# Kernel tuning notes

Hardware: AMD Instinct MI355X
Metric: run time of the kernel (lower is better)

The kernel has to match this reference:

```python
import jax, jax.numpy as jnp
import numpy as np

N_HEADS, D_MODEL, D_HEAD = 16, 1024, 64
BATCH, SEQ = 2, 2048
INIT_RANGE = 0.02


def setup_inputs() -> dict:
    key = jax.random.key(0)
    ks = jax.random.split(key, 5)
    x = jax.random.normal(ks[0], (BATCH, SEQ, D_MODEL), dtype=jnp.float32)
    W_Q = jax.random.normal(ks[1], (N_HEADS, D_MODEL, D_HEAD), dtype=jnp.float32) * INIT_RANGE
    W_K = jax.random.normal(ks[2], (N_HEADS, D_MODEL, D_HEAD), dtype=jnp.float32) * INIT_RANGE
    W_V = jax.random.normal(ks[3], (N_HEADS, D_MODEL, D_HEAD), dtype=jnp.float32) * INIT_RANGE
    W_O = jax.random.normal(ks[4], (N_HEADS, D_HEAD, D_MODEL), dtype=jnp.float32) * INIT_RANGE
    b_Q = jnp.zeros((N_HEADS, D_HEAD), dtype=jnp.float32)
    b_K = jnp.zeros((N_HEADS, D_HEAD), dtype=jnp.float32)
    b_V = jnp.zeros((N_HEADS, D_HEAD), dtype=jnp.float32)
    b_O = jnp.zeros((D_MODEL,), dtype=jnp.float32)
    return {"normalized_resid_pre": x, "W_Q": W_Q, "W_K": W_K, "W_V": W_V,
            "W_O": W_O, "b_Q": b_Q, "b_K": b_K, "b_V": b_V, "b_O": b_O}


def reference(normalized_resid_pre, W_Q, W_K, W_V, W_O, b_Q, b_K, b_V, b_O):
    x = normalized_resid_pre  # [b, s, d_model]
    q = jnp.einsum('bsm,hmd->bshd', x, W_Q) + b_Q  # [b, s, h, d_head]
    k = jnp.einsum('bsm,hmd->bshd', x, W_K) + b_K
    v = jnp.einsum('bsm,hmd->bshd', x, W_V) + b_V
    scores = jnp.einsum('bqhd,bkhd->bhqk', q, k) / jnp.sqrt(jnp.float32(D_HEAD))
    seq = x.shape[1]
    causal = jnp.tril(jnp.ones((seq, seq), dtype=bool))  # True where allowed
    scores = jnp.where(causal, scores, jnp.float32(-jnp.inf))
    pattern = jax.nn.softmax(scores, axis=-1)  # [b, h, q, k]
    z = jnp.einsum('bhqk,bkhd->bqhd', pattern, v)
    attn_out = jnp.einsum('bqhd,hdm->bqm', z, W_O) + b_O
    return attn_out
```

## Files before the change

kernel.cpp:

```cpp
#include <hip/hip_runtime.h>
#include <hip/hip_bf16.h>

#define BATCH 2
#define SEQL 2048
#define NH 16
#define DH 64
#define DM 1024
#define LDK 72
#define QSCALE 0.1803368801111244f

typedef __hip_bfloat16 bf16;
typedef __attribute__((ext_vector_type(8))) short  bf16x8;
typedef __attribute__((ext_vector_type(4))) float  f32x4;

__device__ __forceinline__ void gl_lds16(const void* g, void* l) {
    __builtin_amdgcn_global_load_lds(
        (const __attribute__((address_space(1))) unsigned int*)g,
        (__attribute__((address_space(3))) unsigned int*)l, 16, 0, 0);
}

__global__ __launch_bounds__(256) void prep_kernel(
    const float* __restrict__ x,
    const float* __restrict__ Wq, const float* __restrict__ Wk,
    const float* __restrict__ Wv, const float* __restrict__ Wo,
    bf16* __restrict__ Wt, bf16* __restrict__ xb)
{
    const int zi = blockIdx.z;
    if (zi == 4) {
        const int bid = blockIdx.y * 16 + blockIdx.x;
        const size_t base = ((size_t)bid * 256 + threadIdx.x) * 4;
        #pragma unroll
        for (int it = 0; it < 16; ++it) {
            const size_t i = base + (size_t)it * 262144;
            const float4 v = *(const float4*)(x + i);
            bf16 o[4];
            o[0] = __float2bfloat16(v.x); o[1] = __float2bfloat16(v.y);
            o[2] = __float2bfloat16(v.z); o[3] = __float2bfloat16(v.w);
            *(uint2*)(xb + i) = *(const uint2*)o;
        }
        return;
    }

    __shared__ float ts[64][65];
    const float* src = (zi == 0) ? Wq : (zi == 1) ? Wk : (zi == 2) ? Wv : Wo;
    bf16* dst = Wt + (size_t)zi * DM * DM;
    const int row0 = blockIdx.y * 64;
    const int col0 = blockIdx.x * 64;
    const int tx = threadIdx.x & 63;
    const int ty = threadIdx.x >> 6;

    if (zi < 3) {
        const int h = col0 >> 6;
        #pragma unroll
        for (int i = 0; i < 16; ++i) {
            const int r = ty + 4 * i;
            ts[r][tx] = src[h * (DM * DH) + (row0 + r) * DH + tx];
        }
    } else {
        #pragma unroll
        for (int i = 0; i < 16; ++i) {
            const int r = ty + 4 * i;
            ts[r][tx] = src[(size_t)(row0 + r) * DM + col0 + tx];
        }
    }
    __syncthreads();
    #pragma unroll
    for (int i = 0; i < 16; ++i) {
        const int rr = ty + 4 * i;
        dst[(size_t)(col0 + rr) * DM + row0 + tx] = __float2bfloat16(ts[tx][rr]);
    }
}

__global__ __launch_bounds__(256) void qkv_gemm(
    const bf16* __restrict__ xb, const bf16* __restrict__ Wt,
    const float* __restrict__ bq, const float* __restrict__ bk, const float* __restrict__ bv,
    bf16* __restrict__ qkv)
{
    __shared__ __align__(16) bf16 As[2][128 * 32];
    __shared__ __align__(16) bf16 Bs[2][128 * 32];

    const int t = threadIdx.x;
    const int lane = t & 63, w = t >> 6;
    const int ml = lane & 15, quad = lane >> 4;
    const int wr = w >> 1, wc = w & 1;
    const int bn = blockIdx.x, bm = blockIdx.y, which = blockIdx.z;

    const bf16* A0 = xb + (size_t)(bm * 128) * DM;
    const bf16* B0 = Wt + (size_t)which * DM * DM + (size_t)(bn * 128) * DM;
    const float* bias = (which == 0) ? bq : (which == 1) ? bk : bv;
    bf16* outb = qkv + (size_t)which * (BATCH * SEQL * NH * DH);
    const float oscale = (which == 0) ? QSCALE : 1.0f;

    f32x4 acc[4][4];
    #pragma unroll
    for (int i = 0; i < 4; ++i)
        #pragma unroll
        for (int j = 0; j < 4; ++j) acc[i][j] = (f32x4){0.f, 0.f, 0.f, 0.f};

    const int r0 = t >> 2, c0 = (t & 3) * 8;
    const int f1 = t + 256;
    const int r1 = f1 >> 2, c1 = (f1 & 3) * 8;

    for (int kt = 0; kt < DM / 64; ++kt) {
        const int k0 = kt * 64;
        __syncthreads();
        #pragma unroll
        for (int half = 0; half < 2; ++half) {
            const int kh = k0 + half * 32;
            gl_lds16(A0 + (size_t)r0 * DM + kh + c0, &As[half][t * 8]);
            gl_lds16(A0 + (size_t)r1 * DM + kh + c1, &As[half][f1 * 8]);
            gl_lds16(B0 + (size_t)r0 * DM + kh + c0, &Bs[half][t * 8]);
            gl_lds16(B0 + (size_t)r1 * DM + kh + c1, &Bs[half][f1 * 8]);
        }
        __syncthreads();
        #pragma unroll
        for (int half = 0; half < 2; ++half) {
            bf16x8 af[4], bfr[4];
            #pragma unroll
            for (int i = 0; i < 4; ++i)
                af[i] = *(const bf16x8*)&As[half][(wr * 64 + i * 16 + ml) * 32 + quad * 8];
            #pragma unroll
            for (int j = 0; j < 4; ++j)
                bfr[j] = *(const bf16x8*)&Bs[half][(wc * 64 + j * 16 + ml) * 32 + quad * 8];
            #pragma unroll
            for (int i = 0; i < 4; ++i)
                #pragma unroll
                for (int j = 0; j < 4; ++j)
                    acc[i][j] = __builtin_amdgcn_mfma_f32_16x16x32_bf16(af[i], bfr[j], acc[i][j], 0, 0, 0);
        }
    }

    float bb[4];
    #pragma unroll
    for (int j = 0; j < 4; ++j) bb[j] = bias[bn * 128 + wc * 64 + j * 16 + ml];

    if (which == 2) {
        #pragma unroll
        for (int i = 0; i < 4; ++i) {
            const int row0v = bm * 128 + wr * 64 + i * 16 + quad * 4;
            const int b = row0v >> 11;
            const int s0 = row0v & (SEQL - 1);
            #pragma unroll
            for (int j = 0; j < 4; ++j) {
                const int col = bn * 128 + wc * 64 + j * 16 + ml;
                const int h = col >> 6, d = col & 63;
                bf16 tmp[4];
                #pragma unroll
                for (int rg = 0; rg < 4; ++rg)
                    tmp[rg] = __float2bfloat16(acc[i][j][rg] + bb[j]);
                *(uint2*)&outb[(((size_t)(b * NH + h)) * DH + d) * SEQL + s0] =
                    *(const uint2*)tmp;
            }
        }
    } else {
        #pragma unroll
        for (int i = 0; i < 4; ++i) {
            #pragma unroll
            for (int rg = 0; rg < 4; ++rg) {
                const int row = bm * 128 + wr * 64 + i * 16 + quad * 4 + rg;
                const int b = row >> 11;
                const int s = row & (SEQL - 1);
                #pragma unroll
                for (int j = 0; j < 4; ++j) {
                    const int col = bn * 128 + wc * 64 + j * 16 + ml;
                    const int h = col >> 6, d = col & 63;
                    outb[(((size_t)(b * NH + h)) * SEQL + s) * DH + d] =
                        __float2bfloat16((acc[i][j][rg] + bb[j]) * oscale);
                }
            }
        }
    }
}

__global__ __launch_bounds__(256) void oproj_gemm(
    const bf16* __restrict__ zb, const bf16* __restrict__ Bt,
    const float* __restrict__ bo, float* __restrict__ out)
{
    __shared__ __align__(16) bf16 As[2][128 * 32];
    __shared__ __align__(16) bf16 Bs[2][64 * 32];

    const int t = threadIdx.x;
    const int lane = t & 63, w = t >> 6;
    const int ml = lane & 15, quad = lane >> 4;
    const int wr = w >> 1, wc = w & 1;
    const int bn = blockIdx.x, bm = blockIdx.y;

    const bf16* A0 = zb + (size_t)(bm * 128) * DM;
    const bf16* B0 = Bt + (size_t)(bn * 64) * DM;

    f32x4 acc[4][2];
    #pragma unroll
    for (int i = 0; i < 4; ++i)
        #pragma unroll
        for (int j = 0; j < 2; ++j) acc[i][j] = (f32x4){0.f, 0.f, 0.f, 0.f};

    const int r0 = t >> 2, c0 = (t & 3) * 8;
    const int f1 = t + 256;
    const int r1 = f1 >> 2, c1 = (f1 & 3) * 8;

    for (int kt = 0; kt < DM / 64; ++kt) {
        const int k0 = kt * 64;
        __syncthreads();
        #pragma unroll
        for (int half = 0; half < 2; ++half) {
            const int kh = k0 + half * 32;
            gl_lds16(A0 + (size_t)r0 * DM + kh + c0, &As[half][t * 8]);
            gl_lds16(A0 + (size_t)r1 * DM + kh + c1, &As[half][f1 * 8]);
            gl_lds16(B0 + (size_t)r0 * DM + kh + c0, &Bs[half][t * 8]);
        }
        __syncthreads();
        #pragma unroll
        for (int half = 0; half < 2; ++half) {
            bf16x8 af[4], bfr[2];
            #pragma unroll
            for (int i = 0; i < 4; ++i)
                af[i] = *(const bf16x8*)&As[half][(wr * 64 + i * 16 + ml) * 32 + quad * 8];
            #pragma unroll
            for (int j = 0; j < 2; ++j)
                bfr[j] = *(const bf16x8*)&Bs[half][(wc * 32 + j * 16 + ml) * 32 + quad * 8];
            #pragma unroll
            for (int i = 0; i < 4; ++i)
                #pragma unroll
                for (int j = 0; j < 2; ++j)
                    acc[i][j] = __builtin_amdgcn_mfma_f32_16x16x32_bf16(af[i], bfr[j], acc[i][j], 0, 0, 0);
        }
    }

    float bb[2];
    #pragma unroll
    for (int j = 0; j < 2; ++j) bb[j] = bo[bn * 64 + wc * 32 + j * 16 + ml];

    #pragma unroll
    for (int i = 0; i < 4; ++i) {
        #pragma unroll
        for (int rg = 0; rg < 4; ++rg) {
            const int row = bm * 128 + wr * 64 + i * 16 + quad * 4 + rg;
            #pragma unroll
            for (int j = 0; j < 2; ++j) {
                const int col = bn * 64 + wc * 32 + j * 16 + ml;
                out[(size_t)row * DM + col] = acc[i][j][rg] + bb[j];
            }
        }
    }
}

__global__ __launch_bounds__(512) void attn_kernel(
    const bf16* __restrict__ qg, const bf16* __restrict__ kg, const bf16* __restrict__ vtg,
    bf16* __restrict__ z)
{
    __shared__ __align__(16) bf16 KsS[64 * 64];
    __shared__ __align__(16) bf16 VtS[64 * 64];
    __shared__ __align__(16) bf16 PsS[8][16 * LDK];

    const int t    = threadIdx.x;
    const int lane = t & 63;
    const int w    = t >> 6;
    const int m    = lane & 15;
    const int quad = lane >> 4;
    const int wg   = w & 3;
    const int half = w >> 2;

    const int bh = blockIdx.x;
    const int b  = bh >> 4;
    const int h  = bh & 15;
    const int qa = blockIdx.y;
    const int qb = 31 - qa;
    const int q0a = qa * 64;
    const int q0b = qb * 64;

    const size_t base   = (size_t)bh * SEQL * DH;
    const size_t vtbase = (size_t)bh * DH * SEQL;

    const int s  = t;
    const int rs = s >> 3, cs = (s & 7) ^ (rs & 7);

    bf16x8 aq[2], aqB[2];
    {
        const int myq = (w < 4) ? (q0a + w * 16) : (q0b + wg * 16);
        const bf16* qp = qg + base + (size_t)(myq + m) * DH + quad * 8;
        aq[0] = *(const bf16x8*)(qp);
        aq[1] = *(const bf16x8*)(qp + 32);
        const bf16* qpb = qg + base + (size_t)(q0b + wg * 16 + m) * DH + quad * 8;
        aqB[0] = *(const bf16x8*)(qpb);
        aqB[1] = *(const bf16x8*)(qpb + 32);
    }

    const short ob = (m == 0) ? (short)0x3F80 : (short)0;
    const bf16x8 bones = {ob, ob, ob, ob, ob, ob, ob, ob};

    f32x4 zacc[4];
    #pragma unroll
    for (int nt = 0; nt < 4; ++nt) zacc[nt] = (f32x4){0.f, 0.f, 0.f, 0.f};
    f32x4 lacc = (f32x4){0.f, 0.f, 0.f, 0.f};

    bf16* Psw = PsS[w];

    for (int kt = 0; kt <= qb; ++kt) {
        __syncthreads();
        {
            const int kc = kt * 64;
            gl_lds16(kg + base + (size_t)(kc + rs) * DH + cs * 8, &KsS[s * 8]);
            gl_lds16(vtg + vtbase + (size_t)rs * SEQL + kc + cs * 8, &VtS[s * 8]);
        }
        __syncthreads();

        if (kt <= qa) {
            f32x4 sc[4];
            #pragma unroll
            for (int nt = 0; nt < 4; ++nt) sc[nt] = (f32x4){0.f, 0.f, 0.f, 0.f};
            __builtin_amdgcn_s_setprio(1);
            #pragma unroll
            for (int ks = 0; ks < 2; ++ks) {
                #pragma unroll
                for (int nt = 0; nt < 4; ++nt) {
                    const int row = nt * 16 + m;
                    const int pc  = ((ks << 2) + quad) ^ (m & 7);
                    const bf16x8 bk = *(const bf16x8*)(&KsS[row * 64 + pc * 8]);
                    sc[nt] = __builtin_amdgcn_mfma_f32_16x16x32_bf16(aq[ks], bk, sc[nt], 0, 0, 0);
                }
            }
            __builtin_amdgcn_s_setprio(0);
            if (kt == qa && w < 4) {
                #pragma unroll
                for (int nt = 0; nt < 4; ++nt) {
                    const int col = nt * 16 + m;
                    #pragma unroll
                    for (int rg = 0; rg < 4; ++rg) {
                        const int row = wg * 16 + quad * 4 + rg;
                        if (col > row) sc[nt][rg] = -1e30f;
                    }
                }
            }

            #pragma unroll
            for (int nt = 0; nt < 4; ++nt)
                #pragma unroll
                for (int rg = 0; rg < 4; ++rg)
                    Psw[(quad * 4 + rg) * LDK + nt * 16 + m] =
                        __float2bfloat16(__builtin_exp2f(sc[nt][rg]));

            __builtin_amdgcn_s_setprio(1);
            #pragma unroll
            for (int ks = 0; ks < 2; ++ks) {
                const bf16x8 ap = *(const bf16x8*)(&Psw[m * LDK + ks * 32 + quad * 8]);
                lacc = __builtin_amdgcn_mfma_f32_16x16x32_bf16(ap, bones, lacc, 0, 0, 0);
                #pragma unroll
                for (int nt = 0; nt < 4; ++nt) {
                    const int row = nt * 16 + m;
                    const int pc  = ((ks << 2) + quad) ^ (m & 7);
                    const bf16x8 bv = *(const bf16x8*)(&VtS[row * 64 + pc * 8]);
                    zacc[nt] = __builtin_amdgcn_mfma_f32_16x16x32_bf16(ap, bv, zacc[nt], 0, 0, 0);
                }
            }
            __builtin_amdgcn_s_setprio(0);

            if (kt == qa && w < 4) {
                float invl[4];
                #pragma unroll
                for (int rg = 0; rg < 4; ++rg)
                    invl[rg] = 1.f / __shfl(lacc[rg], quad * 16);
                #pragma unroll
                for (int nt = 0; nt < 4; ++nt) {
                    const int d = nt * 16 + m;
                    #pragma unroll
                    for (int rg = 0; rg < 4; ++rg) {
                        const int qrow = q0a + wg * 16 + quad * 4 + rg;
                        z[(((size_t)b * SEQL + qrow) * NH + h) * DH + d] =
                            __float2bfloat16(zacc[nt][rg] * invl[rg]);
                    }
                }
                #pragma unroll
                for (int nt = 0; nt < 4; ++nt) zacc[nt] = (f32x4){0.f, 0.f, 0.f, 0.f};
                lacc = (f32x4){0.f, 0.f, 0.f, 0.f};
                aq[0] = aqB[0]; aq[1] = aqB[1];
            }
        } else {
            f32x4 sc[2];
            sc[0] = (f32x4){0.f, 0.f, 0.f, 0.f};
            sc[1] = (f32x4){0.f, 0.f, 0.f, 0.f};
            __builtin_amdgcn_s_setprio(1);
            #pragma unroll
            for (int ks = 0; ks < 2; ++ks) {
                #pragma unroll
                for (int nt = 0; nt < 2; ++nt) {
                    const int row = half * 32 + nt * 16 + m;
                    const int pc  = ((ks << 2) + quad) ^ (m & 7);
                    const bf16x8 bk = *(const bf16x8*)(&KsS[row * 64 + pc * 8]);
                    sc[nt] = __builtin_amdgcn_mfma_f32_16x16x32_bf16(aq[ks], bk, sc[nt], 0, 0, 0);
                }
            }
            __builtin_amdgcn_s_setprio(0);
            if (kt == qb) {
                #pragma unroll
                for (int nt = 0; nt < 2; ++nt) {
                    const int col = half * 32 + nt * 16 + m;
                    #pragma unroll
                    for (int rg = 0; rg < 4; ++rg) {
                        const int row = wg * 16 + quad * 4 + rg;
                        if (col > row) sc[nt][rg] = -1e30f;
                    }
                }
            }

            #pragma unroll
            for (int nt = 0; nt < 2; ++nt)
                #pragma unroll
                for (int rg = 0; rg < 4; ++rg)
                    Psw[(quad * 4 + rg) * LDK + nt * 16 + m] =
                        __float2bfloat16(__builtin_exp2f(sc[nt][rg]));

            __builtin_amdgcn_s_setprio(1);
            {
                const bf16x8 ap = *(const bf16x8*)(&Psw[m * LDK + quad * 8]);
                lacc = __builtin_amdgcn_mfma_f32_16x16x32_bf16(ap, bones, lacc, 0, 0, 0);
                #pragma unroll
                for (int nt = 0; nt < 4; ++nt) {
                    const int row = nt * 16 + m;
                    const int pc  = ((half << 2) + quad) ^ (m & 7);
                    const bf16x8 bv = *(const bf16x8*)(&VtS[row * 64 + pc * 8]);
                    zacc[nt] = __builtin_amdgcn_mfma_f32_16x16x32_bf16(ap, bv, zacc[nt], 0, 0, 0);
                }
            }
            __builtin_amdgcn_s_setprio(0);
        }
    }

    __syncthreads();
    if (w < 4) {
        float* zs = (w < 2) ? ((float*)KsS) + (size_t)w * 1024
                            : ((float*)VtS) + (size_t)(w - 2) * 1024;
        #pragma unroll
        for (int nt = 0; nt < 4; ++nt)
            #pragma unroll
            for (int rg = 0; rg < 4; ++rg)
                zs[lane * 16 + nt * 4 + rg] = zacc[nt][rg];
        float* ls = ((float*)PsS) + w * 256;
        #pragma unroll
        for (int rg = 0; rg < 4; ++rg) ls[lane * 4 + rg] = lacc[rg];
    }
    __syncthreads();
    if (w >= 4) {
        const int ww = w - 4;
        const float* zs = (ww < 2) ? ((const float*)KsS) + (size_t)ww * 1024
                                   : ((const float*)VtS) + (size_t)(ww - 2) * 1024;
        const float* ls = ((const float*)PsS) + ww * 256;
        #pragma unroll
        for (int nt = 0; nt < 4; ++nt)
            #pragma unroll
            for (int rg = 0; rg < 4; ++rg)
                zacc[nt][rg] += zs[lane * 16 + nt * 4 + rg];
        #pragma unroll
        for (int rg = 0; rg < 4; ++rg) lacc[rg] += ls[lane * 4 + rg];

        float invl[4];
        #pragma unroll
        for (int rg = 0; rg < 4; ++rg)
            invl[rg] = 1.f / __shfl(lacc[rg], quad * 16);
        #pragma unroll
        for (int nt = 0; nt < 4; ++nt) {
            const int d = nt * 16 + m;
            #pragma unroll
            for (int rg = 0; rg < 4; ++rg) {
                const int qrow = q0b + wg * 16 + quad * 4 + rg;
                z[(((size_t)b * SEQL + qrow) * NH + h) * DH + d] =
                    __float2bfloat16(zacc[nt][rg] * invl[rg]);
            }
        }
    }
}

extern "C" void kernel_launch(void* const* d_in, const int* in_sizes, int n_in,
                              void* d_out, int out_size, void* d_ws, size_t ws_size,
                              hipStream_t stream)
{
    const float* x  = (const float*)d_in[0];
    const float* Wq = (const float*)d_in[1];
    const float* Wk = (const float*)d_in[2];
    const float* Wv = (const float*)d_in[3];
    const float* Wo = (const float*)d_in[4];
    const float* bq = (const float*)d_in[5];
    const float* bk = (const float*)d_in[6];
    const float* bv = (const float*)d_in[7];
    const float* bo = (const float*)d_in[8];
    float* out = (float*)d_out;

    const size_t TOK = (size_t)BATCH * SEQL;
    const size_t QKV = TOK * DM;
    bf16* xb  = (bf16*)d_ws;
    bf16* Wt  = xb + QKV;
    bf16* qkv = Wt + 4 * (size_t)DM * DM;
    bf16* zb  = qkv + 3 * QKV;

    prep_kernel<<<dim3(16, 16, 5), 256, 0, stream>>>(x, Wq, Wk, Wv, Wo, Wt, xb);
    qkv_gemm<<<dim3(8, 32, 3), 256, 0, stream>>>(xb, Wt, bq, bk, bv, qkv);
    attn_kernel<<<dim3(BATCH * NH, 16), 512, 0, stream>>>(
        qkv, qkv + QKV, qkv + 2 * QKV, zb);
    oproj_gemm<<<dim3(16, 32), 256, 0, stream>>>(zb, Wt + 3 * (size_t)DM * DM, bo, out);
}
```

Measured before the change: 184.8 us.

## Restructure QKV GEMM into 256x256 tiles with pipelined swizzled LDS staging

Rewrites the QKV projection GEMM to use 512-thread blocks computing 256x256 output tiles over the concatenated QKV weight. K-slices are staged two ahead into XOR-swizzled LDS buffers, loads are interleaved between MFMA phases, and setprio is raised around the MFMA sections. The block index is remapped so that neighbouring blocks share A and B tiles. The aim is more operand reuse per LDS load, fewer bank conflicts and overlap of global loads with compute, at the cost of much higher register and LDS use (64KB per block) and only 192 blocks launched.

```diff
diff --git a/kernel.cpp b/kernel.cpp
--- a/kernel.cpp
+++ b/kernel.cpp
@@ -10,8 +10,8 @@
 #define QSCALE 0.1803368801111244f
 
 typedef __hip_bfloat16 bf16;
-typedef __attribute__((ext_vector_type(8))) short  bf16x8;
-typedef __attribute__((ext_vector_type(4))) float  f32x4;
+typedef __attribute__((ext_vector_type(8)))  short bf16x8;
+typedef __attribute__((ext_vector_type(4)))  float f32x4;
 
 __device__ __forceinline__ void gl_lds16(const void* g, void* l) {
     __builtin_amdgcn_global_load_lds(
@@ -71,104 +71,195 @@
     }
 }
 
-__global__ __launch_bounds__(256) void qkv_gemm(
+__global__ __launch_bounds__(512, 2) void qkv_gemm(
     const bf16* __restrict__ xb, const bf16* __restrict__ Wt,
     const float* __restrict__ bq, const float* __restrict__ bk, const float* __restrict__ bv,
     bf16* __restrict__ qkv)
 {
-    __shared__ __align__(16) bf16 As[2][128 * 32];
-    __shared__ __align__(16) bf16 Bs[2][128 * 32];
+    __shared__ __align__(16) bf16 As[2][256 * 64];
+    __shared__ __align__(16) bf16 Bs[2][256 * 64];
 
     const int t = threadIdx.x;
     const int lane = t & 63, w = t >> 6;
     const int ml = lane & 15, quad = lane >> 4;
-    const int wr = w >> 1, wc = w & 1;
-    const int bn = blockIdx.x, bm = blockIdx.y, which = blockIdx.z;
-
-    const bf16* A0 = xb + (size_t)(bm * 128) * DM;
-    const bf16* B0 = Wt + (size_t)which * DM * DM + (size_t)(bn * 128) * DM;
+    const int mlx = ml & 7;
+    const int wr = w >> 2, wc = w & 3;
+
+    const int bid0 = blockIdx.y * 12 + blockIdx.x;
+    const int bid  = (bid0 & 7) * 24 + (bid0 >> 3);
+    const int bn = bid % 12, bm = bid / 12;
+
+    const bf16* A0 = xb + (size_t)bm * 256 * DM;
+    const bf16* B0 = Wt + (size_t)bn * 256 * DM;
+
+    const int sr = t >> 3;
+    const int sc = (t & 7) ^ (sr & 7);
+
+#define STG(Xs_buf, X0, h, kk) do {                                           \
+    gl_lds16((X0) + (size_t)((h) * 128 + sr) * DM + (kk) + sc * 8,            \
+             (Xs_buf) + (h) * 8192 + t * 8);                                  \
+    gl_lds16((X0) + (size_t)((h) * 128 + 64 + sr) * DM + (kk) + sc * 8,       \
+             (Xs_buf) + (h) * 8192 + 4096 + t * 8);                           \
+} while (0)
+
+    f32x4 acc[8][4];
+    #pragma unroll
+    for (int i = 0; i < 8; ++i)
+        #pragma unroll
+        for (int j = 0; j < 4; ++j) acc[i][j] = (f32x4){0.f, 0.f, 0.f, 0.f};
+
+    STG(As[0], A0, 0, 0); STG(As[0], A0, 1, 0);
+    STG(Bs[0], B0, 0, 0); STG(Bs[0], B0, 1, 0);
+    STG(As[1], A0, 0, 64); STG(As[1], A0, 1, 64);
+    STG(Bs[1], B0, 0, 64); STG(Bs[1], B0, 1, 64);
+    asm volatile("s_waitcnt vmcnt(8)" ::: "memory");
+    __builtin_amdgcn_s_barrier();
+
+    const int T = DM / 64;
+    for (int kt = 0; kt < T; ++kt) {
+        const int cur = kt & 1;
+        const bf16* Ac = As[cur];
+        const bf16* Bc = Bs[cur];
+        bf16* Asn = As[cur];
+        bf16* Bsn = Bs[cur];
+        const bool st = (kt + 2 < T);
+        const int kk2 = (kt + 2) * 64;
+
+        bf16x8 af[4][2];
+        bf16x8 bfr[2][2][2];
+
+        #pragma unroll
+        for (int i = 0; i < 4; ++i)
+            #pragma unroll
+            for (int ks = 0; ks < 2; ++ks)
+                af[i][ks] = *(const bf16x8*)&Ac[(wr * 64 + i * 16 + ml) * 64 +
+                                                (((ks << 2) + quad) ^ mlx) * 8];
+        #pragma unroll
+        for (int j = 0; j < 2; ++j)
+            #pragma unroll
+            for (int ks = 0; ks < 2; ++ks)
+                bfr[0][j][ks] = *(const bf16x8*)&Bc[(wc * 32 + j * 16 + ml) * 64 +
+                                                    (((ks << 2) + quad) ^ mlx) * 8];
+        __builtin_amdgcn_s_setprio(1);
+        #pragma unroll
+        for (int i = 0; i < 4; ++i)
+            #pragma unroll
+            for (int j = 0; j < 2; ++j)
+                #pragma unroll
+                for (int ks = 0; ks < 2; ++ks)
+                    acc[i][j] = __builtin_amdgcn_mfma_f32_16x16x32_bf16(
+                        af[i][ks], bfr[0][j][ks], acc[i][j], 0, 0, 0);
+        __builtin_amdgcn_s_setprio(0);
+        __builtin_amdgcn_s_barrier();
+
+        #pragma unroll
+        for (int j = 0; j < 2; ++j)
+            #pragma unroll
+            for (int ks = 0; ks < 2; ++ks)
+                bfr[1][j][ks] = *(const bf16x8*)&Bc[(128 + wc * 32 + j * 16 + ml) * 64 +
+                                                    (((ks << 2) + quad) ^ mlx) * 8];
+        if (st) { STG(Asn, A0, 0, kk2); STG(Bsn, B0, 0, kk2); }
+        __builtin_amdgcn_s_setprio(1);
+        #pragma unroll
+        for (int i = 0; i < 4; ++i)
+            #pragma unroll
+            for (int j = 0; j < 2; ++j)
+                #pragma unroll
+                for (int ks = 0; ks < 2; ++ks)
+                    acc[i][2 + j] = __builtin_amdgcn_mfma_f32_16x16x32_bf16(
+                        af[i][ks], bfr[1][j][ks], acc[i][2 + j], 0, 0, 0);
+        __builtin_amdgcn_s_setprio(0);
+        __builtin_amdgcn_s_barrier();
+
+        #pragma unroll
+        for (int i = 0; i < 4; ++i)
+            #pragma unroll
+            for (int ks = 0; ks < 2; ++ks)
+                af[i][ks] = *(const bf16x8*)&Ac[(128 + wr * 64 + i * 16 + ml) * 64 +
+                                                (((ks << 2) + quad) ^ mlx) * 8];
+        if (st) { STG(Bsn, B0, 1, kk2); }
+        __builtin_amdgcn_s_setprio(1);
+        #pragma unroll
+        for (int i = 0; i < 4; ++i)
+            #pragma unroll
+            for (int j = 0; j < 2; ++j)
+                #pragma unroll
+                for (int ks = 0; ks < 2; ++ks)
+                    acc[4 + i][2 + j] = __builtin_amdgcn_mfma_f32_16x16x32_bf16(
+                        af[i][ks], bfr[1][j][ks], acc[4 + i][2 + j], 0, 0, 0);
+        __builtin_amdgcn_s_setprio(0);
+        __builtin_amdgcn_s_barrier();
+
+        if (st) { STG(Asn, A0, 1, kk2); }
+        __builtin_amdgcn_s_setprio(1);
+        #pragma unroll
+        for (int i = 0; i < 4; ++i)
+            #pragma unroll
+            for (int j = 0; j < 2; ++j)
+                #pragma unroll
+                for (int ks = 0; ks < 2; ++ks)
+                    acc[4 + i][j] = __builtin_amdgcn_mfma_f32_16x16x32_bf16(
+                        af[i][ks], bfr[0][j][ks], acc[4 + i][j], 0, 0, 0);
+        __builtin_amdgcn_s_setprio(0);
+
+        if (kt < T - 2) {
+            asm volatile("s_waitcnt vmcnt(8)" ::: "memory");
+        } else if (kt == T - 2) {
+            asm volatile("s_waitcnt vmcnt(0)" ::: "memory");
+        }
+        if (kt < T - 1) __builtin_amdgcn_s_barrier();
+    }
+#undef STG
+
+    const int which = bn >> 2;
     const float* bias = (which == 0) ? bq : (which == 1) ? bk : bv;
     bf16* outb = qkv + (size_t)which * (BATCH * SEQL * NH * DH);
     const float oscale = (which == 0) ? QSCALE : 1.0f;
-
-    f32x4 acc[4][4];
-    #pragma unroll
-    for (int i = 0; i < 4; ++i)
-        #pragma unroll
-        for (int j = 0; j < 4; ++j) acc[i][j] = (f32x4){0.f, 0.f, 0.f, 0.f};
-
-    const int r0 = t >> 2, c0 = (t & 3) * 8;
-    const int f1 = t + 256;
-    const int r1 = f1 >> 2, c1 = (f1 & 3) * 8;
-
-    for (int kt = 0; kt < DM / 64; ++kt) {
-        const int k0 = kt * 64;
-        __syncthreads();
-        #pragma unroll
-        for (int half = 0; half < 2; ++half) {
-            const int kh = k0 + half * 32;
-            gl_lds16(A0 + (size_t)r0 * DM + kh + c0, &As[half][t * 8]);
-            gl_lds16(A0 + (size_t)r1 * DM + kh + c1, &As[half][f1 * 8]);
-            gl_lds16(B0 + (size_t)r0 * DM + kh + c0, &Bs[half][t * 8]);
-            gl_lds16(B0 + (size_t)r1 * DM + kh + c1, &Bs[half][f1 * 8]);
-        }
-        __syncthreads();
-        #pragma unroll
-        for (int half = 0; half < 2; ++half) {
-            bf16x8 af[4], bfr[4];
+    const int colbase = (bn & 3) * 256;
+
+    if (which == 2) {
+        #pragma unroll
+        for (int mh = 0; mh < 2; ++mh)
+            #pragma unroll
+            for (int i = 0; i < 4; ++i) {
+                const int row0v = bm * 256 + mh * 128 + wr * 64 + i * 16 + quad * 4;
+                const int b = row0v >> 11;
+                const int s0 = row0v & (SEQL - 1);
+                #pragma unroll
+                for (int nh = 0; nh < 2; ++nh)
+                    #pragma unroll
+                    for (int j = 0; j < 2; ++j) {
+                        const int cw = colbase + nh * 128 + wc * 32 + j * 16 + ml;
+                        const int h = cw >> 6, d = cw & 63;
+                        const float bb = bias[cw];
+                        bf16 tmp[4];
+                        #pragma unroll
+                        for (int rg = 0; rg < 4; ++rg)
+                            tmp[rg] = __float2bfloat16(acc[mh * 4 + i][nh * 2 + j][rg] + bb);
+                        *(uint2*)&outb[(((size_t)(b * NH + h)) * DH + d) * SEQL + s0] =
+                            *(const uint2*)tmp;
+                    }
+            }
+    } else {
+        #pragma unroll
+        for (int mh = 0; mh < 2; ++mh)
             #pragma unroll
             for (int i = 0; i < 4; ++i)
-                af[i] = *(const bf16x8*)&As[half][(wr * 64 + i * 16 + ml) * 32 + quad * 8];
-            #pragma unroll
-            for (int j = 0; j < 4; ++j)
-                bfr[j] = *(const bf16x8*)&Bs[half][(wc * 64 + j * 16 + ml) * 32 + quad * 8];
-            #pragma unroll
-            for (int i = 0; i < 4; ++i)
-                #pragma unroll
-                for (int j = 0; j < 4; ++j)
-                    acc[i][j] = __builtin_amdgcn_mfma_f32_16x16x32_bf16(af[i], bfr[j], acc[i][j], 0, 0, 0);
-        }
-    }
-
-    float bb[4];
-    #pragma unroll
-    for (int j = 0; j < 4; ++j) bb[j] = bias[bn * 128 + wc * 64 + j * 16 + ml];
-
-    if (which == 2) {
-        #pragma unroll
-        for (int i = 0; i < 4; ++i) {
-            const int row0v = bm * 128 + wr * 64 + i * 16 + quad * 4;
-            const int b = row0v >> 11;
-            const int s0 = row0v & (SEQL - 1);
-            #pragma unroll
-            for (int j = 0; j < 4; ++j) {
-                const int col = bn * 128 + wc * 64 + j * 16 + ml;
-                const int h = col >> 6, d = col & 63;
-                bf16 tmp[4];
-                #pragma unroll
-                for (int rg = 0; rg < 4; ++rg)
-                    tmp[rg] = __float2bfloat16(acc[i][j][rg] + bb[j]);
-                *(uint2*)&outb[(((size_t)(b * NH + h)) * DH + d) * SEQL + s0] =
-                    *(const uint2*)tmp;
-            }
-        }
-    } else {
-        #pragma unroll
-        for (int i = 0; i < 4; ++i) {
-            #pragma unroll
-            for (int rg = 0; rg < 4; ++rg) {
-                const int row = bm * 128 + wr * 64 + i * 16 + quad * 4 + rg;
-                const int b = row >> 11;
-                const int s = row & (SEQL - 1);
-                #pragma unroll
-                for (int j = 0; j < 4; ++j) {
-                    const int col = bn * 128 + wc * 64 + j * 16 + ml;
-                    const int h = col >> 6, d = col & 63;
-                    outb[(((size_t)(b * NH + h)) * SEQL + s) * DH + d] =
-                        __float2bfloat16((acc[i][j][rg] + bb[j]) * oscale);
-                }
-            }
-        }
+                #pragma unroll
+                for (int rg = 0; rg < 4; ++rg) {
+                    const int row = bm * 256 + mh * 128 + wr * 64 + i * 16 + quad * 4 + rg;
+                    const int b = row >> 11;
+                    const int s = row & (SEQL - 1);
+                    #pragma unroll
+                    for (int nh = 0; nh < 2; ++nh)
+                        #pragma unroll
+                        for (int j = 0; j < 2; ++j) {
+                            const int cw = colbase + nh * 128 + wc * 32 + j * 16 + ml;
+                            const int h = cw >> 6, d = cw & 63;
+                            outb[(((size_t)(b * NH + h)) * SEQL + s) * DH + d] =
+                                __float2bfloat16((acc[mh * 4 + i][nh * 2 + j][rg] + bias[cw]) * oscale);
+                        }
+                }
     }
 }
 
@@ -492,7 +583,7 @@
     bf16* zb  = qkv + 3 * QKV;
 
     prep_kernel<<<dim3(16, 16, 5), 256, 0, stream>>>(x, Wq, Wk, Wv, Wo, Wt, xb);
-    qkv_gemm<<<dim3(8, 32, 3), 256, 0, stream>>>(xb, Wt, bq, bk, bv, qkv);
+    qkv_gemm<<<dim3(12, 16), 512, 0, stream>>>(xb, Wt, bq, bk, bv, qkv);
     attn_kernel<<<dim3(BATCH * NH, 16), 512, 0, stream>>>(
         qkv, qkv + QKV, qkv + 2 * QKV, zb);
     oproj_gemm<<<dim3(16, 32), 256, 0, stream>>>(zb, Wt + 3 * (size_t)DM * DM, bo, out);
```

Result: no change. 187.7 us (+1.6%).

## Load 128-key K/V chunks per barrier pair in attention kernel

Applied to the files above, without the earlier changes.

The attention loop now stages two 64-key tiles (128 keys) of K and transposed V into shared memory per iteration and processes them in an inner two-step loop. This halves the number of __syncthreads pairs and global-to-LDS load phases. The V tile uses a 16-way XOR swizzle over 128 columns. In exchange, LDS use grows, which may lower occupancy, and the final odd tile can load unused keys past qb.

```diff
diff --git a/kernel.cpp b/kernel.cpp
--- a/kernel.cpp
+++ b/kernel.cpp
@@ -10,8 +10,8 @@
 #define QSCALE 0.1803368801111244f
 
 typedef __hip_bfloat16 bf16;
-typedef __attribute__((ext_vector_type(8))) short  bf16x8;
-typedef __attribute__((ext_vector_type(4))) float  f32x4;
+typedef __attribute__((ext_vector_type(8)))  short bf16x8;
+typedef __attribute__((ext_vector_type(4)))  float f32x4;
 
 __device__ __forceinline__ void gl_lds16(const void* g, void* l) {
     __builtin_amdgcn_global_load_lds(
@@ -248,8 +248,8 @@
     const bf16* __restrict__ qg, const bf16* __restrict__ kg, const bf16* __restrict__ vtg,
     bf16* __restrict__ z)
 {
-    __shared__ __align__(16) bf16 KsS[64 * 64];
-    __shared__ __align__(16) bf16 VtS[64 * 64];
+    __shared__ __align__(16) bf16 KsS[128 * 64];
+    __shared__ __align__(16) bf16 VtS[64 * 128];
     __shared__ __align__(16) bf16 PsS[8][16 * LDK];
 
     const int t    = threadIdx.x;
@@ -271,8 +271,11 @@
     const size_t base   = (size_t)bh * SEQL * DH;
     const size_t vtbase = (size_t)bh * DH * SEQL;
 
-    const int s  = t;
-    const int rs = s >> 3, cs = (s & 7) ^ (rs & 7);
+    const int s0 = t, s1 = t + 512;
+    const int kr0 = s0 >> 3, kc0 = (s0 & 7) ^ (kr0 & 7);
+    const int kr1 = s1 >> 3, kc1 = (s1 & 7) ^ (kr1 & 7);
+    const int vr0 = s0 >> 4, vc0 = (s0 & 15) ^ (vr0 & 15);
+    const int vr1 = s1 >> 4, vc1 = (s1 & 15) ^ (vr1 & 15);
 
     bf16x8 aq[2], aqB[2];
     {
@@ -295,133 +298,143 @@
 
     bf16* Psw = PsS[w];
 
-    for (int kt = 0; kt <= qb; ++kt) {
+    const int CB = (qb >> 1) + 1;
+    for (int c = 0; c < CB; ++c) {
         __syncthreads();
         {
-            const int kc = kt * 64;
-            gl_lds16(kg + base + (size_t)(kc + rs) * DH + cs * 8, &KsS[s * 8]);
-            gl_lds16(vtg + vtbase + (size_t)rs * SEQL + kc + cs * 8, &VtS[s * 8]);
+            const int kc = c * 128;
+            gl_lds16(kg + base + (size_t)(kc + kr0) * DH + kc0 * 8, &KsS[s0 * 8]);
+            gl_lds16(kg + base + (size_t)(kc + kr1) * DH + kc1 * 8, &KsS[s1 * 8]);
+            gl_lds16(vtg + vtbase + (size_t)vr0 * SEQL + kc + vc0 * 8, &VtS[s0 * 8]);
+            gl_lds16(vtg + vtbase + (size_t)vr1 * SEQL + kc + vc1 * 8, &VtS[s1 * 8]);
         }
         __syncthreads();
 
-        if (kt <= qa) {
-            f32x4 sc[4];
-            #pragma unroll
-            for (int nt = 0; nt < 4; ++nt) sc[nt] = (f32x4){0.f, 0.f, 0.f, 0.f};
-            __builtin_amdgcn_s_setprio(1);
-            #pragma unroll
-            for (int ks = 0; ks < 2; ++ks) {
-                #pragma unroll
-                for (int nt = 0; nt < 4; ++nt) {
-                    const int row = nt * 16 + m;
-                    const int pc  = ((ks << 2) + quad) ^ (m & 7);
-                    const bf16x8 bk = *(const bf16x8*)(&KsS[row * 64 + pc * 8]);
-                    sc[nt] = __builtin_amdgcn_mfma_f32_16x16x32_bf16(aq[ks], bk, sc[nt], 0, 0, 0);
-                }
+        #pragma unroll
+        for (int c2 = 0; c2 < 2; ++c2) {
+            const int kt = 2 * c + c2;
+            if (kt > qb) break;
+            const int co = c2 * 64;
+
+            if (kt <= qa) {
+                f32x4 sc[4];
+                #pragma unroll
+                for (int nt = 0; nt < 4; ++nt) sc[nt] = (f32x4){0.f, 0.f, 0.f, 0.f};
+                __builtin_amdgcn_s_setprio(1);
+                #pragma unroll
+                for (int ks = 0; ks < 2; ++ks) {
+                    #pragma unroll
+                    for (int nt = 0; nt < 4; ++nt) {
+                        const int rw = co + nt * 16 + m;
+                        const int pc = ((ks << 2) + quad) ^ (m & 7);
+                        const bf16x8 bk = *(const bf16x8*)(&KsS[rw * 64 + pc * 8]);
+                        sc[nt] = __builtin_amdgcn_mfma_f32_16x16x32_bf16(aq[ks], bk, sc[nt], 0, 0, 0);
+                    }
+                }
+                __builtin_amdgcn_s_setprio(0);
+                if (kt == qa && w < 4) {
+                    #pragma unroll
+                    for (int nt = 0; nt < 4; ++nt) {
+                        const int col = nt * 16 + m;
+                        #pragma unroll
+                        for (int rg = 0; rg < 4; ++rg) {
+                            const int row = wg * 16 + quad * 4 + rg;
+                            if (col > row) sc[nt][rg] = -1e30f;
+                        }
+                    }
+                }
+
+                #pragma unroll
+                for (int nt = 0; nt < 4; ++nt)
+                    #pragma unroll
+                    for (int rg = 0; rg < 4; ++rg)
+                        Psw[(quad * 4 + rg) * LDK + nt * 16 + m] =
+                            __float2bfloat16(__builtin_exp2f(sc[nt][rg]));
+
+                __builtin_amdgcn_s_setprio(1);
+                #pragma unroll
+                for (int ks = 0; ks < 2; ++ks) {
+                    const bf16x8 ap = *(const bf16x8*)(&Psw[m * LDK + ks * 32 + quad * 8]);
+                    lacc = __builtin_amdgcn_mfma_f32_16x16x32_bf16(ap, bones, lacc, 0, 0, 0);
+                    #pragma unroll
+                    for (int nt = 0; nt < 4; ++nt) {
+                        const int dr = nt * 16 + m;
+                        const int vc = (c2 * 8 + (ks << 2) + quad) ^ m;
+                        const bf16x8 bv = *(const bf16x8*)(&VtS[dr * 128 + vc * 8]);
+                        zacc[nt] = __builtin_amdgcn_mfma_f32_16x16x32_bf16(ap, bv, zacc[nt], 0, 0, 0);
+                    }
+                }
+                __builtin_amdgcn_s_setprio(0);
+
+                if (kt == qa && w < 4) {
+                    float invl[4];
+                    #pragma unroll
+                    for (int rg = 0; rg < 4; ++rg)
+                        invl[rg] = 1.f / __shfl(lacc[rg], quad * 16);
+                    #pragma unroll
+                    for (int nt = 0; nt < 4; ++nt) {
+                        const int d = nt * 16 + m;
+                        #pragma unroll
+                        for (int rg = 0; rg < 4; ++rg) {
+                            const int qrow = q0a + wg * 16 + quad * 4 + rg;
+                            z[(((size_t)b * SEQL + qrow) * NH + h) * DH + d] =
+                                __float2bfloat16(zacc[nt][rg] * invl[rg]);
+                        }
+                    }
+                    #pragma unroll
+                    for (int nt = 0; nt < 4; ++nt) zacc[nt] = (f32x4){0.f, 0.f, 0.f, 0.f};
+                    lacc = (f32x4){0.f, 0.f, 0.f, 0.f};
+                    aq[0] = aqB[0]; aq[1] = aqB[1];
+                }
+            } else {
+                f32x4 sc[2];
+                sc[0] = (f32x4){0.f, 0.f, 0.f, 0.f};
+                sc[1] = (f32x4){0.f, 0.f, 0.f, 0.f};
+                __builtin_amdgcn_s_setprio(1);
+                #pragma unroll
+                for (int ks = 0; ks < 2; ++ks) {
+                    #pragma unroll
+                    for (int nt = 0; nt < 2; ++nt) {
+                        const int rw = co + half * 32 + nt * 16 + m;
+                        const int pc = ((ks << 2) + quad) ^ (m & 7);
+                        const bf16x8 bk = *(const bf16x8*)(&KsS[rw * 64 + pc * 8]);
+                        sc[nt] = __builtin_amdgcn_mfma_f32_16x16x32_bf16(aq[ks], bk, sc[nt], 0, 0, 0);
+                    }
+                }
+                __builtin_amdgcn_s_setprio(0);
+                if (kt == qb) {
+                    #pragma unroll
+                    for (int nt = 0; nt < 2; ++nt) {
+                        const int col = half * 32 + nt * 16 + m;
+                        #pragma unroll
+                        for (int rg = 0; rg < 4; ++rg) {
+                            const int row = wg * 16 + quad * 4 + rg;
+                            if (col > row) sc[nt][rg] = -1e30f;
+                        }
+                    }
+                }
+
+                #pragma unroll
+                for (int nt = 0; nt < 2; ++nt)
+                    #pragma unroll
+                    for (int rg = 0; rg < 4; ++rg)
+                        Psw[(quad * 4 + rg) * LDK + nt * 16 + m] =
+                            __float2bfloat16(__builtin_exp2f(sc[nt][rg]));
+
+                __builtin_amdgcn_s_setprio(1);
+                {
+                    const bf16x8 ap = *(const bf16x8*)(&Psw[m * LDK + quad * 8]);
+                    lacc = __builtin_amdgcn_mfma_f32_16x16x32_bf16(ap, bones, lacc, 0, 0, 0);
+                    #pragma unroll
+                    for (int nt = 0; nt < 4; ++nt) {
+                        const int dr = nt * 16 + m;
+                        const int vc = (c2 * 8 + (half << 2) + quad) ^ m;
+                        const bf16x8 bv = *(const bf16x8*)(&VtS[dr * 128 + vc * 8]);
+                        zacc[nt] = __builtin_amdgcn_mfma_f32_16x16x32_bf16(ap, bv, zacc[nt], 0, 0, 0);
+                    }
+                }
+                __builtin_amdgcn_s_setprio(0);
             }
-            __builtin_amdgcn_s_setprio(0);
-            if (kt == qa && w < 4) {
-                #pragma unroll
-                for (int nt = 0; nt < 4; ++nt) {
-                    const int col = nt * 16 + m;
-                    #pragma unroll
-                    for (int rg = 0; rg < 4; ++rg) {
-                        const int row = wg * 16 + quad * 4 + rg;
-                        if (col > row) sc[nt][rg] = -1e30f;
-                    }
-                }
-            }
-
-            #pragma unroll
-            for (int nt = 0; nt < 4; ++nt)
-                #pragma unroll
-                for (int rg = 0; rg < 4; ++rg)
-                    Psw[(quad * 4 + rg) * LDK + nt * 16 + m] =
-                        __float2bfloat16(__builtin_exp2f(sc[nt][rg]));
-
-            __builtin_amdgcn_s_setprio(1);
-            #pragma unroll
-            for (int ks = 0; ks < 2; ++ks) {
-                const bf16x8 ap = *(const bf16x8*)(&Psw[m * LDK + ks * 32 + quad * 8]);
-                lacc = __builtin_amdgcn_mfma_f32_16x16x32_bf16(ap, bones, lacc, 0, 0, 0);
-                #pragma unroll
-                for (int nt = 0; nt < 4; ++nt) {
-                    const int row = nt * 16 + m;
-                    const int pc  = ((ks << 2) + quad) ^ (m & 7);
-                    const bf16x8 bv = *(const bf16x8*)(&VtS[row * 64 + pc * 8]);
-                    zacc[nt] = __builtin_amdgcn_mfma_f32_16x16x32_bf16(ap, bv, zacc[nt], 0, 0, 0);
-                }
-            }
-            __builtin_amdgcn_s_setprio(0);
-
-            if (kt == qa && w < 4) {
-                float invl[4];
-                #pragma unroll
-                for (int rg = 0; rg < 4; ++rg)
-                    invl[rg] = 1.f / __shfl(lacc[rg], quad * 16);
-                #pragma unroll
-                for (int nt = 0; nt < 4; ++nt) {
-                    const int d = nt * 16 + m;
-                    #pragma unroll
-                    for (int rg = 0; rg < 4; ++rg) {
-                        const int qrow = q0a + wg * 16 + quad * 4 + rg;
-                        z[(((size_t)b * SEQL + qrow) * NH + h) * DH + d] =
-                            __float2bfloat16(zacc[nt][rg] * invl[rg]);
-                    }
-                }
-                #pragma unroll
-                for (int nt = 0; nt < 4; ++nt) zacc[nt] = (f32x4){0.f, 0.f, 0.f, 0.f};
-                lacc = (f32x4){0.f, 0.f, 0.f, 0.f};
-                aq[0] = aqB[0]; aq[1] = aqB[1];
-            }
-        } else {
-            f32x4 sc[2];
-            sc[0] = (f32x4){0.f, 0.f, 0.f, 0.f};
-            sc[1] = (f32x4){0.f, 0.f, 0.f, 0.f};
-            __builtin_amdgcn_s_setprio(1);
-            #pragma unroll
-            for (int ks = 0; ks < 2; ++ks) {
-                #pragma unroll
-                for (int nt = 0; nt < 2; ++nt) {
-                    const int row = half * 32 + nt * 16 + m;
-                    const int pc  = ((ks << 2) + quad) ^ (m & 7);
-                    const bf16x8 bk = *(const bf16x8*)(&KsS[row * 64 + pc * 8]);
-                    sc[nt] = __builtin_amdgcn_mfma_f32_16x16x32_bf16(aq[ks], bk, sc[nt], 0, 0, 0);
-                }
-            }
-            __builtin_amdgcn_s_setprio(0);
-            if (kt == qb) {
-                #pragma unroll
-                for (int nt = 0; nt < 2; ++nt) {
-                    const int col = half * 32 + nt * 16 + m;
-                    #pragma unroll
-                    for (int rg = 0; rg < 4; ++rg) {
-                        const int row = wg * 16 + quad * 4 + rg;
-                        if (col > row) sc[nt][rg] = -1e30f;
-                    }
-                }
-            }
-
-            #pragma unroll
-            for (int nt = 0; nt < 2; ++nt)
-                #pragma unroll
-                for (int rg = 0; rg < 4; ++rg)
-                    Psw[(quad * 4 + rg) * LDK + nt * 16 + m] =
-                        __float2bfloat16(__builtin_exp2f(sc[nt][rg]));
-
-            __builtin_amdgcn_s_setprio(1);
-            {
-                const bf16x8 ap = *(const bf16x8*)(&Psw[m * LDK + quad * 8]);
-                lacc = __builtin_amdgcn_mfma_f32_16x16x32_bf16(ap, bones, lacc, 0, 0, 0);
-                #pragma unroll
-                for (int nt = 0; nt < 4; ++nt) {
-                    const int row = nt * 16 + m;
-                    const int pc  = ((half << 2) + quad) ^ (m & 7);
-                    const bf16x8 bv = *(const bf16x8*)(&VtS[row * 64 + pc * 8]);
-                    zacc[nt] = __builtin_amdgcn_mfma_f32_16x16x32_bf16(ap, bv, zacc[nt], 0, 0, 0);
-                }
-            }
-            __builtin_amdgcn_s_setprio(0);
         }
     }
 
```

Result: no change. 182.3 us (-1.3%).
